# Kernel optimization log

Hardware: AMD Instinct MI355X
Metric: run time of the kernel (lower is better)

## Reference

```python
import jax, jax.numpy as jnp
import numpy as np

N, D, K = 262144, 64, 64
TEMPERATURE = 1.0
PRIOR_P = 0.1
PRIOR_LOGVAR0 = -2.0  # prior_logvar_0 buffer (constant per-dim)
LOG2PI = float(np.log(2.0 * np.pi))


def setup_inputs() -> dict:
    key = jax.random.key(0)
    k1, k2, k3, k4 = jax.random.split(key, 4)
    prior_phi_probs = jnp.full((D,), PRIOR_P, dtype=jnp.float32)
    phi_logits = jnp.log(prior_phi_probs / (1.0 - prior_phi_probs))  # init = prior log-odds
    return {
        "X": jax.random.normal(k1, (N, D), dtype=jnp.float32),
        "u_noise": jax.random.uniform(k2, (D,), dtype=jnp.float32),
        "phi_logits": phi_logits,
        "q_mu": jax.random.normal(k3, (K, D), dtype=jnp.float32),
        "q_logvar": jnp.full((K, D), -1.0, dtype=jnp.float32),
        "pi_logits": jnp.ones((K,), dtype=jnp.float32),
        "prior_phi_probs": prior_phi_probs,
    }


def reference(X, u_noise, phi_logits, q_mu, q_logvar, pi_logits, prior_phi_probs):
    n = X.shape[0]
    # Gumbel-sigmoid sample of phi (per-dimension gate), shape (D,)
    gumbel = -jnp.log(-jnp.log(u_noise + 1e-9) + 1e-9)
    phi = jax.nn.sigmoid((phi_logits + gumbel) / TEMPERATURE)

    logvar = jnp.clip(q_logvar, -5.0, 5.0)            # (K, D)
    inv_var = jnp.exp(-logvar)                        # (K, D)

    # sum_d phi_d * log N(x_d | mu_kd, var_kd), decomposed to GEMM form so the
    # full (N, K, D) tensor is never materialized:
    #   -0.5 * [ sum_d phi*(LOG2PI + logvar_kd)  +  sum_d phi*(x-mu)^2/var_kd ]
    a = phi[None, :] * inv_var                        # (K, D)
    quad = (jnp.einsum('nd,kd->nk', X * X, a)
            - 2.0 * jnp.einsum('nd,kd->nk', X, q_mu * a)
            + jnp.sum(q_mu * q_mu * a, axis=1)[None, :])          # (N, K)
    const_k = jnp.sum(phi[None, :] * (LOG2PI + logvar), axis=1)   # (K,)
    lp_cluster = -0.5 * (const_k[None, :] + quad)                 # (N, K)

    # background term: sum_d (1-phi_d) * log N(x_d | 0, exp(prior_logvar_0)); per-sample scalar
    inv_var0 = float(np.exp(-PRIOR_LOGVAR0))
    lp_bg = -0.5 * jnp.sum((1.0 - phi)[None, :]
                           * (LOG2PI + PRIOR_LOGVAR0 + X * X * inv_var0), axis=1)  # (N,)

    log_p_x_given_z = lp_cluster + lp_bg[:, None]     # (N, K)

    pi = jax.nn.softmax(pi_logits)
    log_joint = log_p_x_given_z + jnp.log(pi + 1e-9)[None, :]
    log_likelihood = jnp.sum(jax.nn.logsumexp(log_joint, axis=1))

    q_phi = jnp.clip(jax.nn.sigmoid(phi_logits), 1e-6, 1.0 - 1e-6)
    p_phi = jnp.clip(prior_phi_probs, 1e-6, 1.0 - 1e-6)
    kl_phi = jnp.sum(q_phi * (jnp.log(q_phi) - jnp.log(p_phi))
                     + (1.0 - q_phi) * (jnp.log(1.0 - q_phi) - jnp.log(1.0 - p_phi))) * n

    loss = -log_likelihood + kl_phi
    return (loss, q_phi, log_p_x_given_z)
```

## Files before the change

kernel.cpp:

```cpp
#include <hip/hip_runtime.h>
#include <hip/hip_bf16.h>
#include <math.h>

#define N_SAMPLES 262144
#define DDIM 64
#define KDIM 64
#define NBLOCKS 4096
#define NPART (NBLOCKS * 4)

#define LOG2PI 1.8378770664093453f
#define PRIOR_LV0 -2.0f
#define IV0 7.389056098930650f


#define WS_C     4096
#define WS_CL    4160
#define WS_PART  4224
#define WS_KL    (WS_PART + NPART)

typedef __attribute__((ext_vector_type(8))) short short8;
typedef __attribute__((ext_vector_type(4))) float floatx4;

static __device__ inline unsigned short f2bf_bits(float f) {
  union { float f; unsigned u; } v; v.f = f;
  unsigned r = v.u + 0x7fffu + ((v.u >> 16) & 1u);
  return (unsigned short)(r >> 16);
}

__global__ __launch_bounds__(256) void setup_frags(
    const float* __restrict__ u_noise, const float* __restrict__ phi_logits,
    const float* __restrict__ q_mu, const float* __restrict__ q_logvar,
    const float* __restrict__ pi_logits, const float* __restrict__ prior_p,
    float* __restrict__ out, float* __restrict__ ws) {
  __shared__ float sPhi[DDIM];
  __shared__ float sR[DDIM];
  __shared__ float sLpi[KDIM];
  __shared__ float sBeta;
  __shared__ float sPart[4][KDIM];
  int tid = threadIdx.x;

  if (tid < 64) {
    int d = tid;
    float u = u_noise[d];
    float g = -__logf(-__logf(u + 1e-9f) + 1e-9f);
    float phi = 1.0f / (1.0f + __expf(-(phi_logits[d] + g)));
    sPhi[d] = phi;
    sR[d] = -0.5f * (1.0f - phi) * IV0;

    float betap = -0.5f * (1.0f - phi) * (LOG2PI + PRIOR_LV0);
    #pragma unroll
    for (int o = 1; o < 64; o <<= 1) betap += __shfl_xor(betap, o, 64);
    if (d == 0) sBeta = betap;

    float l = pi_logits[d];
    float m = l;
    #pragma unroll
    for (int o = 1; o < 64; o <<= 1) m = fmaxf(m, __shfl_xor(m, o, 64));
    float e = __expf(l - m);
    float s = e;
    #pragma unroll
    for (int o = 1; o < 64; o <<= 1) s += __shfl_xor(s, o, 64);
    sLpi[d] = __logf(e / s + 1e-9f);
  } else if (tid >= 64 && tid < 128) {
    int d = tid - 64;
    float qp = 1.0f / (1.0f + __expf(-phi_logits[d]));
    qp = fminf(fmaxf(qp, 1e-6f), 1.0f - 1e-6f);
    out[1 + d] = qp;
    float pp = fminf(fmaxf(prior_p[d], 1e-6f), 1.0f - 1e-6f);
    float klp = qp * (__logf(qp) - __logf(pp)) +
                (1.0f - qp) * (__logf(1.0f - qp) - __logf(1.0f - pp));
    #pragma unroll
    for (int o = 1; o < 64; o <<= 1) klp += __shfl_xor(klp, o, 64);
    if (d == 0) ws[WS_KL] = klp * (float)N_SAMPLES;
  }
  __syncthreads();

  {
    int k = tid & 63, seg = tid >> 6;
    const float* lvp = q_logvar + k * DDIM + seg * 16;
    const float* mup = q_mu + k * DDIM + seg * 16;
    float ap = 0.0f;
    #pragma unroll
    for (int dd = 0; dd < 16; ++dd) {
      int d = seg * 16 + dd;
      float lv = fminf(fmaxf(lvp[dd], -5.0f), 5.0f);
      float mu = mup[dd];
      ap += sPhi[d] * (LOG2PI + lv) + mu * mu * sPhi[d] * __expf(-lv);
    }
    sPart[seg][k] = ap;
  }

  unsigned short* bsw = (unsigned short*)ws;
  #pragma unroll
  for (int p = 0; p < 4; ++p) {
    int pr = p * 256 + tid;
    int s = pr >> 6, l = pr & 63;
    int kc = s >> 2, tl = s & 3, q = l >> 4, nn = l & 15;
    int k = tl * 16 + nn;
    int dbase = (kc & 1) * 32 + q * 8;
    const float* lvp = q_logvar + k * DDIM + dbase;
    float4 lv0 = *(const float4*)lvp;
    float4 lv1 = *(const float4*)(lvp + 4);
    float lvv[8] = {lv0.x, lv0.y, lv0.z, lv0.w, lv1.x, lv1.y, lv1.z, lv1.w};
    short r8[8];
    if (kc < 2) {
      #pragma unroll
      for (int j = 0; j < 8; ++j) {
        int d = dbase + j;
        float lv = fminf(fmaxf(lvv[j], -5.0f), 5.0f);
        r8[j] = (short)f2bf_bits(-0.5f * sPhi[d] * __expf(-lv) + sR[d]);
      }
    } else {
      const float* mup = q_mu + k * DDIM + dbase;
      float4 mu0 = *(const float4*)mup;
      float4 mu1 = *(const float4*)(mup + 4);
      float muv[8] = {mu0.x, mu0.y, mu0.z, mu0.w, mu1.x, mu1.y, mu1.z, mu1.w};
      #pragma unroll
      for (int j = 0; j < 8; ++j) {
        int d = dbase + j;
        float lv = fminf(fmaxf(lvv[j], -5.0f), 5.0f);
        r8[j] = (short)f2bf_bits(muv[j] * sPhi[d] * __expf(-lv));
      }
    }
    ((short8*)bsw)[pr] = (short8){r8[0], r8[1], r8[2], r8[3],
                                  r8[4], r8[5], r8[6], r8[7]};
  }

  __syncthreads();
  if (tid < 64) {
    float alpha = sPart[0][tid] + sPart[1][tid] + sPart[2][tid] + sPart[3][tid];
    float c = -0.5f * alpha + sBeta;
    ws[WS_C + tid] = c;
    ws[WS_CL + tid] = c + sLpi[tid];
  }
}

__global__ __launch_bounds__(256, 8) void gmm_main(
    const float* __restrict__ X, const float* __restrict__ ws,
    float* __restrict__ out) {
  int tid  = threadIdx.x;
  int lane = tid & 63;
  int w    = tid >> 6;
  int n    = lane & 15;
  int q    = lane >> 4;
  long rbase = ((long)blockIdx.x * 4 + w) * 16;

  const float* xr = X + (rbase + n) * DDIM;
  float4 xa0 = *(const float4*)(xr + q * 8);
  float4 xa1 = *(const float4*)(xr + q * 8 + 4);
  float4 xb0 = *(const float4*)(xr + 32 + q * 8);
  float4 xb1 = *(const float4*)(xr + 32 + q * 8 + 4);

  short8 a[4];
  {
    float xa[8] = {xa0.x, xa0.y, xa0.z, xa0.w, xa1.x, xa1.y, xa1.z, xa1.w};
    float xb[8] = {xb0.x, xb0.y, xb0.z, xb0.w, xb1.x, xb1.y, xb1.z, xb1.w};
    #pragma unroll
    for (int j = 0; j < 8; ++j) {
      a[0][j] = (short)f2bf_bits(xa[j] * xa[j]);
      a[1][j] = (short)f2bf_bits(xb[j] * xb[j]);
      a[2][j] = (short)f2bf_bits(xa[j]);
      a[3][j] = (short)f2bf_bits(xb[j]);
    }
  }

  const short8* Bf = (const short8*)ws;
  floatx4 acc[4];
  #pragma unroll
  for (int t = 0; t < 4; ++t) acc[t] = (floatx4){0.f, 0.f, 0.f, 0.f};
  #pragma unroll
  for (int kc = 0; kc < 4; ++kc) {
    #pragma unroll
    for (int t = 0; t < 4; ++t) {
      short8 b = Bf[(kc * 4 + t) * 64 + lane];
      acc[t] = __builtin_amdgcn_mfma_f32_16x16x32_bf16(b, a[kc], acc[t], 0, 0, 0);
    }
  }

  float* lp = out + 1 + DDIM;
  long rowoff = (rbase + n) * KDIM;
  #pragma unroll
  for (int t = 0; t < 4; ++t) {
    float4 cb = *(const float4*)(ws + WS_C  + t * 16 + q * 4);
    float4 cl = *(const float4*)(ws + WS_CL + t * 16 + q * 4);
    float o4[4];
    o4[0] = acc[t][0] + cb.x;
    o4[1] = acc[t][1] + cb.y;
    o4[2] = acc[t][2] + cb.z;
    o4[3] = acc[t][3] + cb.w;
    __builtin_memcpy(lp + rowoff + t * 16 + q * 4, o4, 16);
    acc[t][0] += cl.x;
    acc[t][1] += cl.y;
    acc[t][2] += cl.z;
    acc[t][3] += cl.w;
  }

  float m = acc[0][0];
  #pragma unroll
  for (int t = 0; t < 4; ++t)
    #pragma unroll
    for (int r = 0; r < 4; ++r) m = fmaxf(m, acc[t][r]);
  m = fmaxf(m, __shfl_xor(m, 16, 64));
  m = fmaxf(m, __shfl_xor(m, 32, 64));

  float s = 0.0f;
  #pragma unroll
  for (int t = 0; t < 4; ++t)
    #pragma unroll
    for (int r = 0; r < 4; ++r) s += __expf(acc[t][r] - m);
  s += __shfl_xor(s, 16, 64);
  s += __shfl_xor(s, 32, 64);

  float lse = m + __logf(s);
  lse += __shfl_xor(lse, 1, 64);
  lse += __shfl_xor(lse, 2, 64);
  lse += __shfl_xor(lse, 4, 64);
  lse += __shfl_xor(lse, 8, 64);
  if (lane == 0) {
    float* wsp = (float*)ws;
    wsp[WS_PART + blockIdx.x * 4 + w] = lse;
  }
}

__global__ __launch_bounds__(256) void finalize_kernel(
    const float* __restrict__ ws, float* __restrict__ out) {
  __shared__ float sW[4];
  int tid = threadIdx.x;
  int lane = tid & 63, w = tid >> 6;

  float s = 0.0f;
  #pragma unroll
  for (int i = 0; i < NPART / 256; ++i)
    s += ws[WS_PART + i * 256 + tid];
  #pragma unroll
  for (int o = 1; o < 64; o <<= 1) s += __shfl_xor(s, o, 64);
  if (lane == 0) sW[w] = s;
  __syncthreads();
  if (tid == 0) out[0] = ws[WS_KL] - (sW[0] + sW[1] + sW[2] + sW[3]);
}

extern "C" void kernel_launch(void* const* d_in, const int* in_sizes, int n_in,
                              void* d_out, int out_size, void* d_ws, size_t ws_size,
                              hipStream_t stream) {
  const float* X           = (const float*)d_in[0];
  const float* u_noise     = (const float*)d_in[1];
  const float* phi_logits  = (const float*)d_in[2];
  const float* q_mu        = (const float*)d_in[3];
  const float* q_logvar    = (const float*)d_in[4];
  const float* pi_logits   = (const float*)d_in[5];
  const float* prior_p     = (const float*)d_in[6];
  float* out = (float*)d_out;
  float* ws  = (float*)d_ws;

  setup_frags<<<1, 256, 0, stream>>>(u_noise, phi_logits, q_mu, q_logvar,
                                     pi_logits, prior_p, out, ws);
  gmm_main<<<NBLOCKS, 256, 0, stream>>>(X, ws, out);
  finalize_kernel<<<1, 256, 0, stream>>>(ws, out);
}
```

Measured before the change: 143.4 us.

## Fuse finalize into main kernel via last-block ticket and stage B in LDS

Removes the separate finalize kernel launch. Each block now reduces its four wave partials in shared memory, publishes one partial, and takes an atomic ticket; the last block sums all partials and writes the loss. The B fragments and per-cluster constants are also staged into LDS once per block instead of being read from global memory by every wave. This saves a kernel launch and some redundant global reads, in exchange for extra block-level syncs, about 16KB of LDS per block (which may limit occupancy), and an atomic.

```diff
diff --git a/kernel.cpp b/kernel.cpp
--- a/kernel.cpp
+++ b/kernel.cpp
@@ -6,17 +6,18 @@
 #define DDIM 64
 #define KDIM 64
 #define NBLOCKS 4096
-#define NPART (NBLOCKS * 4)
+#define NPART NBLOCKS
 
 #define LOG2PI 1.8378770664093453f
 #define PRIOR_LV0 -2.0f
 #define IV0 7.389056098930650f
 
 
-#define WS_C     4096
-#define WS_CL    4160
-#define WS_PART  4224
-#define WS_KL    (WS_PART + NPART)
+#define WS_C      4096
+#define WS_CL     4160
+#define WS_PART   4224
+#define WS_KL     (WS_PART + NPART)
+#define WS_TICKET (WS_KL + 1)
 
 typedef __attribute__((ext_vector_type(8))) short short8;
 typedef __attribute__((ext_vector_type(4))) float floatx4;
@@ -38,6 +39,8 @@
   __shared__ float sBeta;
   __shared__ float sPart[4][KDIM];
   int tid = threadIdx.x;
+
+  if (tid == 0) *(unsigned*)(ws + WS_TICKET) = 0u;
 
   if (tid < 64) {
     int d = tid;
@@ -136,8 +139,13 @@
 }
 
 __global__ __launch_bounds__(256, 8) void gmm_main(
-    const float* __restrict__ X, const float* __restrict__ ws,
+    const float* __restrict__ X, float* __restrict__ ws,
     float* __restrict__ out) {
+  __shared__ short8 sB[1024];
+  __shared__ float sCB[KDIM];
+  __shared__ float sCL[KDIM];
+  __shared__ float sW[4];
+  __shared__ int sLast;
   int tid  = threadIdx.x;
   int lane = tid & 63;
   int w    = tid >> 6;
@@ -145,11 +153,19 @@
   int q    = lane >> 4;
   long rbase = ((long)blockIdx.x * 4 + w) * 16;
 
-  const float* xr = X + (rbase + n) * DDIM;
-  float4 xa0 = *(const float4*)(xr + q * 8);
-  float4 xa1 = *(const float4*)(xr + q * 8 + 4);
-  float4 xb0 = *(const float4*)(xr + 32 + q * 8);
-  float4 xb1 = *(const float4*)(xr + 32 + q * 8 + 4);
+  const float* xr = X + (rbase + n) * DDIM + q * 8;
+  float4 xa0 = *(const float4*)(xr);
+  float4 xa1 = *(const float4*)(xr + 4);
+  float4 xb0 = *(const float4*)(xr + 32);
+  float4 xb1 = *(const float4*)(xr + 36);
+
+  {
+    const short8* Bf = (const short8*)ws;
+    #pragma unroll
+    for (int p = 0; p < 4; ++p) sB[p * 256 + tid] = Bf[p * 256 + tid];
+    if (tid < KDIM) { sCB[tid] = ws[WS_C + tid]; sCL[tid] = ws[WS_CL + tid]; }
+  }
+  __syncthreads();
 
   short8 a[4];
   {
@@ -164,7 +180,6 @@
     }
   }
 
-  const short8* Bf = (const short8*)ws;
   floatx4 acc[4];
   #pragma unroll
   for (int t = 0; t < 4; ++t) acc[t] = (floatx4){0.f, 0.f, 0.f, 0.f};
@@ -172,7 +187,7 @@
   for (int kc = 0; kc < 4; ++kc) {
     #pragma unroll
     for (int t = 0; t < 4; ++t) {
-      short8 b = Bf[(kc * 4 + t) * 64 + lane];
+      short8 b = sB[(kc * 4 + t) * 64 + lane];
       acc[t] = __builtin_amdgcn_mfma_f32_16x16x32_bf16(b, a[kc], acc[t], 0, 0, 0);
     }
   }
@@ -181,8 +196,8 @@
   long rowoff = (rbase + n) * KDIM;
   #pragma unroll
   for (int t = 0; t < 4; ++t) {
-    float4 cb = *(const float4*)(ws + WS_C  + t * 16 + q * 4);
-    float4 cl = *(const float4*)(ws + WS_CL + t * 16 + q * 4);
+    float4 cb = *(const float4*)&sCB[t * 16 + q * 4];
+    float4 cl = *(const float4*)&sCL[t * 16 + q * 4];
     float o4[4];
     o4[0] = acc[t][0] + cb.x;
     o4[1] = acc[t][1] + cb.y;
@@ -216,27 +231,33 @@
   lse += __shfl_xor(lse, 2, 64);
   lse += __shfl_xor(lse, 4, 64);
   lse += __shfl_xor(lse, 8, 64);
-  if (lane == 0) {
-    float* wsp = (float*)ws;
-    wsp[WS_PART + blockIdx.x * 4 + w] = lse;
-  }
-}
-
-__global__ __launch_bounds__(256) void finalize_kernel(
-    const float* __restrict__ ws, float* __restrict__ out) {
-  __shared__ float sW[4];
-  int tid = threadIdx.x;
-  int lane = tid & 63, w = tid >> 6;
-
-  float s = 0.0f;
-  #pragma unroll
-  for (int i = 0; i < NPART / 256; ++i)
-    s += ws[WS_PART + i * 256 + tid];
-  #pragma unroll
-  for (int o = 1; o < 64; o <<= 1) s += __shfl_xor(s, o, 64);
-  if (lane == 0) sW[w] = s;
-  __syncthreads();
-  if (tid == 0) out[0] = ws[WS_KL] - (sW[0] + sW[1] + sW[2] + sW[3]);
+  if (lane == 0) sW[w] = lse;
+  __syncthreads();
+
+  if (tid == 0) {
+    float part = sW[0] + sW[1] + sW[2] + sW[3];
+    __hip_atomic_store(&ws[WS_PART + blockIdx.x], part,
+                       __ATOMIC_RELEASE, __HIP_MEMORY_SCOPE_AGENT);
+    unsigned old = __hip_atomic_fetch_add((unsigned*)(ws + WS_TICKET), 1u,
+                                          __ATOMIC_ACQ_REL,
+                                          __HIP_MEMORY_SCOPE_AGENT);
+    sLast = (old == NBLOCKS - 1) ? 1 : 0;
+  }
+  __syncthreads();
+
+  if (sLast) {
+    float t2 = 0.0f;
+    #pragma unroll
+    for (int i = 0; i < NPART / 256; ++i)
+      t2 += __hip_atomic_load(&ws[WS_PART + i * 256 + tid],
+                              __ATOMIC_RELAXED, __HIP_MEMORY_SCOPE_AGENT);
+    #pragma unroll
+    for (int o = 1; o < 64; o <<= 1) t2 += __shfl_xor(t2, o, 64);
+    __syncthreads();
+    if (lane == 0) sW[w] = t2;
+    __syncthreads();
+    if (tid == 0) out[0] = ws[WS_KL] - (sW[0] + sW[1] + sW[2] + sW[3]);
+  }
 }
 
 extern "C" void kernel_launch(void* const* d_in, const int* in_sizes, int n_in,
@@ -255,5 +276,4 @@
   setup_frags<<<1, 256, 0, stream>>>(u_noise, phi_logits, q_mu, q_logvar,
                                      pi_logits, prior_p, out, ws);
   gmm_main<<<NBLOCKS, 256, 0, stream>>>(X, ws, out);
-  finalize_kernel<<<1, 256, 0, stream>>>(ws, out);
-}
+}
```

Result: slower. 501.0 us (+249.3%).
